# Performance work log

Hardware: AMD Instinct MI355X
Metric: run time of the kernel (lower is better)

The kernel has to match this reference:

```python
import jax, jax.numpy as jnp
import numpy as np

EPS = 1e-5  # torch BatchNorm2d default


def _signature_depth3(path):
    """Truncated (depth-3) path signature via Chen's relation.
    path: [B, P, ch] (P points). Returns [B, ch + ch^2 + ch^3] in signatory
    layout (level 1, then row-major flattened levels 2 and 3)."""
    dx = path[:, 1:] - path[:, :-1]  # [B, P-1, ch] increments
    B, _, ch = dx.shape

    def step(carry, v):
        s1, s2, s3 = carry  # [B,ch], [B,ch,ch], [B,ch,ch,ch]
        vv = v[:, :, None] * v[:, None, :]          # v (x) v
        e2 = 0.5 * vv                               # v^(x)2 / 2!
        e3 = vv[:, :, :, None] * v[:, None, None, :] / 6.0  # v^(x)3 / 3!
        n1 = s1 + v
        n2 = s2 + s1[:, :, None] * v[:, None, :] + e2
        n3 = (s3
              + s2[:, :, :, None] * v[:, None, None, :]
              + s1[:, :, None, None] * e2[:, None, :, :]
              + e3)
        return (n1, n2, n3), None

    init = (jnp.zeros((B, ch), dx.dtype),
            jnp.zeros((B, ch, ch), dx.dtype),
            jnp.zeros((B, ch, ch, ch), dx.dtype))
    (s1, s2, s3), _ = jax.lax.scan(step, init, jnp.transpose(dx, (1, 0, 2)))
    return jnp.concatenate([s1, s2.reshape(B, -1), s3.reshape(B, -1)], axis=1)


def setup_inputs() -> dict:
    key = jax.random.key(0)
    ks = jax.random.split(key, 5)
    N, C, J, T, L = 16, 64, 25, 128, 9
    sic, out_dim = 8, 64
    ch = sic + 1                      # +1 time channel
    sig_ch = ch + ch**2 + ch**3       # 819
    x = jax.random.normal(ks[0], (N, C, J, T, L), jnp.float32)
    conv_w = jax.random.normal(ks[1], (sic, C), jnp.float32) * 0.1
    conv_b = jax.random.normal(ks[2], (sic,), jnp.float32) * 0.1
    bn_gamma = jnp.ones((sic,), jnp.float32)
    bn_beta = jnp.zeros((sic,), jnp.float32)
    lin_w = jax.random.normal(ks[3], (out_dim, sig_ch), jnp.float32) * 0.03
    lin_b = jax.random.normal(ks[4], (out_dim,), jnp.float32) * 0.03
    return dict(x=x, conv_w=conv_w, conv_b=conv_b, bn_gamma=bn_gamma,
                bn_beta=bn_beta, lin_w=lin_w, lin_b=lin_b)


def reference(x, conv_w, conv_b, bn_gamma, bn_beta, lin_w, lin_b):
    N, C, J, T, L = x.shape
    # 1x1 conv over channel dim (applied to [N*L, C, J, T] in torch, which is
    # the same per-position linear map)
    y = jnp.einsum('ncjtl,oc->nojtl', x, conv_w) + conv_b[None, :, None, None, None]
    y = jax.nn.relu(y)
    # BatchNorm2d (training mode): stats over all dims except channel
    mean = y.mean(axis=(0, 2, 3, 4), keepdims=True)
    var = ((y - mean) ** 2).mean(axis=(0, 2, 3, 4), keepdims=True)
    y = ((y - mean) * jax.lax.rsqrt(var + EPS)
         * bn_gamma[None, :, None, None, None] + bn_beta[None, :, None, None, None])
    # -> [N*J*T, L, sic] stream per (n, joint, frame)
    B = N * J * T
    p = jnp.transpose(y, (0, 2, 3, 4, 1)).reshape(B, L, -1)
    # signatory.Augment(include_time=True): prepend time channel in [0, 1]
    t = jnp.broadcast_to(jnp.linspace(0.0, 1.0, L, dtype=x.dtype)[None, :, None], (B, L, 1))
    p = jnp.concatenate([t, p], axis=-1)  # [B, L, ch]
    # signature(..., basepoint=True): prepend zero point
    path = jnp.concatenate([jnp.zeros((B, 1, p.shape[-1]), p.dtype), p], axis=1)
    sig = _signature_depth3(path)          # [B, 819]
    z = sig @ lin_w.T + lin_b              # [B, out_dim]
    return jnp.transpose(z.reshape(N, J, T, -1), (0, 3, 1, 2))  # [N, C, J, T]
```

## Files before the change

kernel.cpp:

```cpp
#include <hip/hip_runtime.h>
#include <hip/hip_bf16.h>

typedef unsigned short u16;
typedef __attribute__((ext_vector_type(8))) short short8;
typedef __attribute__((ext_vector_type(4))) float f32x4;

#define N_    16
#define C_    64
#define J_    25
#define T_    128
#define L_    9
#define SIC   8
#define OUT_  64
#define BTOT  (N_*J_*T_)
#define CNT   (BTOT*L_)
#define KPAD  896
#define NKS   27
#define SPB   28

#define K1C_BLOCKS 900
#define K1BT_BLOCKS 224
#define BT_ELEMS (OUT_*KPAD)

#define PART_OFF  0
#define SS_OFF    16384
#define BT_OFF    32768
#define Y_OFF     65536
#define WS_NEED   ((size_t)(Y_OFF + BTOT*72) * 4)

__device__ __forceinline__ short to_bf16(float x) {
  union { __hip_bfloat16 h; u16 u; } cv;
  cv.h = __float2bfloat16(x);
  return (short)cv.u;
}

__global__ __launch_bounds__(256) void k1_conv(
    const float* __restrict__ x, const float* __restrict__ cw,
    const float* __restrict__ cb, const float* __restrict__ lw,
    float* __restrict__ yws, float* __restrict__ part, u16* __restrict__ Bt) {
  int tid = threadIdx.x;

  if (blockIdx.x >= K1C_BLOCKS) {
    int idx = (blockIdx.x - K1C_BLOCKS) * 256 + tid;
    if (idx < BT_ELEMS) {
      int o = idx / KPAD, k = idx % KPAD;
      float v = 0.f;
      if (k < 864) {
        int i = k / 96, p = k % 96;
        if (p < 91) {
          int orig = (p == 0) ? i : (p < 10 ? 9 + i * 9 + (p - 1) : 90 + i * 81 + (p - 10));
          v = lw[o * 819 + orig];
        }
      }
      Bt[idx] = (u16)to_bf16(v);
    }
    return;
  }

  __shared__ float wlT[C_ * SIC];
  __shared__ float bl[SIC];
  __shared__ float wsum[4][16];
  wlT[tid] = cw[(tid & 7) * C_ + (tid >> 3)];
  wlT[tid + 256] = cw[(tid & 7) * C_ + ((tid + 256) >> 3)];
  if (tid < SIC) bl[tid] = cb[tid];
  __syncthreads();

  int p0 = (blockIdx.x * 256 + tid) * 2;
  int n = p0 / 28800, rem = p0 % 28800;
  int jj = rem / 1152, tl0 = rem % 1152;
  const float* xp = x + (size_t)(n * 1600 + jj) * 1152 + tl0;

  float acc[2][8];
#pragma unroll
  for (int p = 0; p < 2; p++)
#pragma unroll
    for (int o = 0; o < 8; o++) acc[p][o] = bl[o];

#pragma unroll 8
  for (int c = 0; c < C_; c++) {
    float2 xv = *(const float2*)(xp + (size_t)c * 28800);
    float4 w0 = *(const float4*)&wlT[c * 8];
    float4 w1 = *(const float4*)&wlT[c * 8 + 4];
    acc[0][0] = fmaf(xv.x, w0.x, acc[0][0]); acc[1][0] = fmaf(xv.y, w0.x, acc[1][0]);
    acc[0][1] = fmaf(xv.x, w0.y, acc[0][1]); acc[1][1] = fmaf(xv.y, w0.y, acc[1][1]);
    acc[0][2] = fmaf(xv.x, w0.z, acc[0][2]); acc[1][2] = fmaf(xv.y, w0.z, acc[1][2]);
    acc[0][3] = fmaf(xv.x, w0.w, acc[0][3]); acc[1][3] = fmaf(xv.y, w0.w, acc[1][3]);
    acc[0][4] = fmaf(xv.x, w1.x, acc[0][4]); acc[1][4] = fmaf(xv.y, w1.x, acc[1][4]);
    acc[0][5] = fmaf(xv.x, w1.y, acc[0][5]); acc[1][5] = fmaf(xv.y, w1.y, acc[1][5]);
    acc[0][6] = fmaf(xv.x, w1.z, acc[0][6]); acc[1][6] = fmaf(xv.y, w1.z, acc[1][6]);
    acc[0][7] = fmaf(xv.x, w1.w, acc[0][7]); acc[1][7] = fmaf(xv.y, w1.w, acc[1][7]);
  }

  float vals[16];
#pragma unroll
  for (int q = 0; q < 16; q++) vals[q] = 0.f;
  float4* dst = (float4*)(yws + (size_t)p0 * 8);
#pragma unroll
  for (int p = 0; p < 2; p++) {
#pragma unroll
    for (int o = 0; o < 8; o++) acc[p][o] = fmaxf(acc[p][o], 0.f);
    dst[p * 2]     = make_float4(acc[p][0], acc[p][1], acc[p][2], acc[p][3]);
    dst[p * 2 + 1] = make_float4(acc[p][4], acc[p][5], acc[p][6], acc[p][7]);
#pragma unroll
    for (int o = 0; o < 8; o++) {
      vals[o] += acc[p][o];
      vals[8 + o] += acc[p][o] * acc[p][o];
    }
  }

  int lane = tid & 63, wid = tid >> 6;
#pragma unroll
  for (int v = 0; v < 16; v++) {
    float s = vals[v];
    for (int off = 32; off > 0; off >>= 1) s += __shfl_down(s, off, 64);
    if (lane == 0) wsum[wid][v] = s;
  }
  __syncthreads();
  if (tid < 16)
    part[blockIdx.x * 16 + tid] = wsum[0][tid] + wsum[1][tid] + wsum[2][tid] + wsum[3][tid];
}

__global__ __launch_bounds__(256) void k2_stats(
    const float* __restrict__ part, const float* __restrict__ gamma,
    const float* __restrict__ beta, float* __restrict__ ss) {
  __shared__ float red[16][16];
  int tid = threadIdx.x;
  int val = tid & 15, grp = tid >> 4;
  float s0 = 0.f, s1 = 0.f, s2 = 0.f, s3 = 0.f;
  int b = grp;
  for (; b + 48 < K1C_BLOCKS; b += 64) {
    s0 += part[b * 16 + val];
    s1 += part[(b + 16) * 16 + val];
    s2 += part[(b + 32) * 16 + val];
    s3 += part[(b + 48) * 16 + val];
  }
  for (; b < K1C_BLOCKS; b += 16) s0 += part[b * 16 + val];
  red[grp][val] = (s0 + s1) + (s2 + s3);
  __syncthreads();
  if (tid < 16) {
    float tot = 0.f;
#pragma unroll
    for (int g = 0; g < 16; g++) tot += red[g][tid];
    red[0][tid] = tot;
  }
  __syncthreads();
  if (tid < 8) {
    float mean = red[0][tid] * (1.f / CNT);
    float var  = red[0][8 + tid] * (1.f / CNT) - mean * mean;
    float sc = gamma[tid] * rsqrtf(var + 1e-5f);
    ss[tid] = sc;
    ss[8 + tid] = beta[tid] - mean * sc;
  }
}

__global__ __launch_bounds__(256, 3) void k3_fused(
    const float* __restrict__ yws, const float* __restrict__ ss,
    const u16* __restrict__ Bt, const float* __restrict__ lb,
    float* __restrict__ out) {
  __shared__ __align__(16) u16 sig_lds[29 * KPAD];
  __shared__ float ssl[16];
  __shared__ float lbl[64];
  float* ylds = (float*)sig_lds;
  int tid = threadIdx.x;
  if (tid < 16) ssl[tid] = ss[tid];
  if (tid >= 64 && tid < 128) lbl[tid - 64] = lb[tid - 64];
  int gBase = blockIdx.x * SPB;
  int valid = BTOT - gBase; if (valid > SPB) valid = SPB;
  __syncthreads();

  if (tid < SPB * 9) {
    int s = tid / 9;
    if (s < valid) {
      const float4* src = (const float4*)(yws + (size_t)gBase * 72 + (size_t)tid * 8);
      float4 a = src[0], b = src[1];
      float* drow = ylds + tid * 8;
      drow[0] = fmaf(a.x, ssl[0], ssl[8]);
      drow[1] = fmaf(a.y, ssl[1], ssl[9]);
      drow[2] = fmaf(a.z, ssl[2], ssl[10]);
      drow[3] = fmaf(a.w, ssl[3], ssl[11]);
      drow[4] = fmaf(b.x, ssl[4], ssl[12]);
      drow[5] = fmaf(b.y, ssl[5], ssl[13]);
      drow[6] = fmaf(b.z, ssl[6], ssl[14]);
      drow[7] = fmaf(b.w, ssl[7], ssl[15]);
    }
  }
  {
    short8 z = {0, 0, 0, 0, 0, 0, 0, 0};
    int padChunks = (29 - valid) * 112;
    for (int e = tid; e < padChunks; e += 256) {
      int r = valid + e / 112, sl = e % 112;
      *(short8*)&sig_lds[r * KPAD + sl * 8] = z;
    }
  }
  __syncthreads();

  int s = tid / 9, i = tid % 9;
  bool act = (tid < SPB * 9) && (s < valid);
  float s1 = 0.f, s2[9], s3[81];
#pragma unroll
  for (int jj = 0; jj < 9; jj++) s2[jj] = 0.f;
#pragma unroll
  for (int q = 0; q < 81; q++) s3[q] = 0.f;
  if (act) {
    const float* yrow = ylds + s * 72;
    int i1 = (i == 0) ? 0 : (i - 1);
    float prev[8], prevvi = 0.f;
#pragma unroll
    for (int c = 0; c < 8; c++) prev[c] = 0.f;

#pragma unroll 3
    for (int l = 0; l < 9; l++) {
      float4 a4 = *(const float4*)(yrow + l * 8);
      float4 b4 = *(const float4*)(yrow + l * 8 + 4);
      float ldsv = yrow[l * 8 + i1];
      float cur[8] = {a4.x, a4.y, a4.z, a4.w, b4.x, b4.y, b4.z, b4.w};
      float v[9];
      v[0] = (l == 0) ? 0.f : 0.125f;
#pragma unroll
      for (int c = 0; c < 8; c++) v[c + 1] = cur[c] - prev[c];
      float curvi = (i == 0) ? (float)l * 0.125f : ldsv;
      float vi = curvi - prevvi;
      prevvi = curvi;
      float aa = fmaf(vi, (1.f / 6.f), 0.5f * s1);
      float b2 = fmaf(vi, 0.5f, s1);
#pragma unroll
      for (int jj = 0; jj < 9; jj++) {
        float tj = fmaf(aa, v[jj], s2[jj]);
#pragma unroll
        for (int k = 0; k < 9; k++) s3[jj * 9 + k] = fmaf(tj, v[k], s3[jj * 9 + k]);
        s2[jj] = fmaf(b2, v[jj], s2[jj]);
      }
      s1 += vi;
#pragma unroll
      for (int c = 0; c < 8; c++) prev[c] = cur[c];
    }
  }
  __syncthreads();

  if (act) {
    u16* rowbase = sig_lds + s * KPAD;
    int sw = s & 7;
    {
      short8 ch;
      ch[0] = to_bf16(s1);
#pragma unroll
      for (int w = 0; w < 7; w++) ch[w + 1] = to_bf16(s2[w]);
      *(short8*)&rowbase[(((i * 12 + 0) ^ sw) * 8)] = ch;
    }
    {
      short8 ch;
      ch[0] = to_bf16(s2[7]); ch[1] = to_bf16(s2[8]);
#pragma unroll
      for (int w = 0; w < 6; w++) ch[w + 2] = to_bf16(s3[w]);
      *(short8*)&rowbase[(((i * 12 + 1) ^ sw) * 8)] = ch;
    }
#pragma unroll
    for (int c = 2; c <= 10; c++) {
      short8 ch;
#pragma unroll
      for (int w = 0; w < 8; w++) ch[w] = to_bf16(s3[c * 8 - 10 + w]);
      *(short8*)&rowbase[(((i * 12 + c) ^ sw) * 8)] = ch;
    }
    {
      short8 ch;
      ch[0] = to_bf16(s3[78]); ch[1] = to_bf16(s3[79]); ch[2] = to_bf16(s3[80]);
      ch[3] = 0; ch[4] = 0; ch[5] = 0; ch[6] = 0; ch[7] = 0;
      *(short8*)&rowbase[(((i * 12 + 11) ^ sw) * 8)] = ch;
    }
  }
  __syncthreads();

  int w = tid >> 6, l = tid & 63;
  int brow = (w << 4) + (l & 15);
  const short8* bp = (const short8*)(Bt + (size_t)brow * KPAD);
  int arow0 = (l & 15);
  int arow1 = 16 + (l & 15); if (arow1 > 28) arow1 = 28;
  int asw0 = arow0 & 7, asw1 = arow1 & 7;
  f32x4 acc0 = {0, 0, 0, 0}, acc1 = {0, 0, 0, 0};
#pragma unroll
  for (int ks = 0; ks < NKS; ks++) {
    int s4 = ks * 4 + (l >> 4);
    short8 bfrag = bp[s4];
    short8 a0 = *(const short8*)&sig_lds[arow0 * KPAD + ((s4 ^ asw0) * 8)];
    short8 a1 = *(const short8*)&sig_lds[arow1 * KPAD + ((s4 ^ asw1) * 8)];
    acc0 = __builtin_amdgcn_mfma_f32_16x16x32_bf16(a0, bfrag, acc0, 0, 0, 0);
    acc1 = __builtin_amdgcn_mfma_f32_16x16x32_bf16(a1, bfrag, acc1, 0, 0, 0);
  }
  __syncthreads();

  float* c_lds = (float*)sig_lds;
  int o = (w << 4) + (l & 15);
#pragma unroll
  for (int r = 0; r < 4; r++) {
    int m0 = (l >> 4) * 4 + r;
    c_lds[o * 33 + m0] = acc0[r];
    c_lds[o * 33 + 16 + m0] = acc1[r];
  }
  __syncthreads();
  for (int e = tid; e < 2048; e += 256) {
    int o2 = e >> 5, m = e & 31;
    if (m < valid) {
      int b = gBase + m;
      int n = b / (J_ * T_), rem = b % (J_ * T_);
      int j = rem >> 7, t = rem & (T_ - 1);
      out[(((size_t)n * OUT_ + o2) * J_ + j) * T_ + t] = c_lds[o2 * 33 + m] + lbl[o2];
    }
  }
}

extern "C" void kernel_launch(void* const* d_in, const int* in_sizes, int n_in,
                              void* d_out, int out_size, void* d_ws, size_t ws_size,
                              hipStream_t stream) {
  const float* x     = (const float*)d_in[0];
  const float* cw    = (const float*)d_in[1];
  const float* cb    = (const float*)d_in[2];
  const float* gamma = (const float*)d_in[3];
  const float* beta  = (const float*)d_in[4];
  const float* lw    = (const float*)d_in[5];
  const float* lbias = (const float*)d_in[6];
  float* out = (float*)d_out;
  float* ws  = (float*)d_ws;
  if (ws_size < WS_NEED) return;

  float* part = ws + PART_OFF;
  float* ss   = ws + SS_OFF;
  u16*   bt   = (u16*)(ws + BT_OFF);
  float* yws  = ws + Y_OFF;

  hipLaunchKernelGGL(k1_conv, dim3(K1C_BLOCKS + K1BT_BLOCKS), dim3(256), 0, stream,
                     x, cw, cb, lw, yws, part, bt);
  hipLaunchKernelGGL(k2_stats, dim3(1), dim3(256), 0, stream, part, gamma, beta, ss);

  int nblk3 = (BTOT + SPB - 1) / SPB;
  hipLaunchKernelGGL(k3_fused, dim3(nblk3), dim3(256), 0, stream, yws, ss, bt, lbias, out);
}
```

Measured before the change: 70.82 us.

## Halve conv block size, use nontemporal x loads and packed bf16 conversion

```diff
diff --git a/kernel.cpp b/kernel.cpp
--- a/kernel.cpp
+++ b/kernel.cpp
@@ -4,6 +4,8 @@
 typedef unsigned short u16;
 typedef __attribute__((ext_vector_type(8))) short short8;
 typedef __attribute__((ext_vector_type(4))) float f32x4;
+typedef __attribute__((ext_vector_type(2))) float f32x2;
+typedef __attribute__((ext_vector_type(4))) unsigned int u32x4;
 
 #define N_    16
 #define C_    64
@@ -18,15 +20,22 @@
 #define NKS   27
 #define SPB   28
 
-#define K1C_BLOCKS 900
-#define K1BT_BLOCKS 224
-#define BT_ELEMS (OUT_*KPAD)
+#define K1_TPB     128
+#define K1C_BLOCKS 1800
+#define BT_ELEMS   (OUT_*KPAD)
+#define K1BT_BLOCKS (BT_ELEMS / K1_TPB)
 
 #define PART_OFF  0
-#define SS_OFF    16384
-#define BT_OFF    32768
-#define Y_OFF     65536
+#define SS_OFF    32768
+#define BT_OFF    40960
+#define Y_OFF     69632
 #define WS_NEED   ((size_t)(Y_OFF + BTOT*72) * 4)
+
+__device__ __forceinline__ unsigned pkbf(float a, float b) {
+  unsigned r;
+  asm("v_cvt_pk_bf16_f32 %0, %1, %2" : "=v"(r) : "v"(a), "v"(b));
+  return r;
+}
 
 __device__ __forceinline__ short to_bf16(float x) {
   union { __hip_bfloat16 h; u16 u; } cv;
@@ -34,38 +43,36 @@
   return (short)cv.u;
 }
 
-__global__ __launch_bounds__(256) void k1_conv(
+__global__ __launch_bounds__(K1_TPB) void k1_conv(
     const float* __restrict__ x, const float* __restrict__ cw,
     const float* __restrict__ cb, const float* __restrict__ lw,
     float* __restrict__ yws, float* __restrict__ part, u16* __restrict__ Bt) {
   int tid = threadIdx.x;
 
   if (blockIdx.x >= K1C_BLOCKS) {
-    int idx = (blockIdx.x - K1C_BLOCKS) * 256 + tid;
-    if (idx < BT_ELEMS) {
-      int o = idx / KPAD, k = idx % KPAD;
-      float v = 0.f;
-      if (k < 864) {
-        int i = k / 96, p = k % 96;
-        if (p < 91) {
-          int orig = (p == 0) ? i : (p < 10 ? 9 + i * 9 + (p - 1) : 90 + i * 81 + (p - 10));
-          v = lw[o * 819 + orig];
-        }
+    int idx = (blockIdx.x - K1C_BLOCKS) * K1_TPB + tid;
+    int o = idx / KPAD, k = idx % KPAD;
+    float v = 0.f;
+    if (k < 864) {
+      int i = k / 96, p = k % 96;
+      if (p < 91) {
+        int orig = (p == 0) ? i : (p < 10 ? 9 + i * 9 + (p - 1) : 90 + i * 81 + (p - 10));
+        v = lw[o * 819 + orig];
       }
-      Bt[idx] = (u16)to_bf16(v);
-    }
+    }
+    Bt[idx] = (u16)to_bf16(v);
     return;
   }
 
   __shared__ float wlT[C_ * SIC];
   __shared__ float bl[SIC];
-  __shared__ float wsum[4][16];
-  wlT[tid] = cw[(tid & 7) * C_ + (tid >> 3)];
-  wlT[tid + 256] = cw[(tid & 7) * C_ + ((tid + 256) >> 3)];
+  __shared__ float wsum[2][16];
+  for (int q = tid; q < C_ * SIC; q += K1_TPB)
+    wlT[q] = cw[(q & 7) * C_ + (q >> 3)];
   if (tid < SIC) bl[tid] = cb[tid];
   __syncthreads();
 
-  int p0 = (blockIdx.x * 256 + tid) * 2;
+  int p0 = (blockIdx.x * K1_TPB + tid) * 2;
   int n = p0 / 28800, rem = p0 % 28800;
   int jj = rem / 1152, tl0 = rem % 1152;
   const float* xp = x + (size_t)(n * 1600 + jj) * 1152 + tl0;
@@ -78,17 +85,17 @@
 
 #pragma unroll 8
   for (int c = 0; c < C_; c++) {
-    float2 xv = *(const float2*)(xp + (size_t)c * 28800);
+    f32x2 xv = __builtin_nontemporal_load((const f32x2*)(xp + (size_t)c * 28800));
     float4 w0 = *(const float4*)&wlT[c * 8];
     float4 w1 = *(const float4*)&wlT[c * 8 + 4];
-    acc[0][0] = fmaf(xv.x, w0.x, acc[0][0]); acc[1][0] = fmaf(xv.y, w0.x, acc[1][0]);
-    acc[0][1] = fmaf(xv.x, w0.y, acc[0][1]); acc[1][1] = fmaf(xv.y, w0.y, acc[1][1]);
-    acc[0][2] = fmaf(xv.x, w0.z, acc[0][2]); acc[1][2] = fmaf(xv.y, w0.z, acc[1][2]);
-    acc[0][3] = fmaf(xv.x, w0.w, acc[0][3]); acc[1][3] = fmaf(xv.y, w0.w, acc[1][3]);
-    acc[0][4] = fmaf(xv.x, w1.x, acc[0][4]); acc[1][4] = fmaf(xv.y, w1.x, acc[1][4]);
-    acc[0][5] = fmaf(xv.x, w1.y, acc[0][5]); acc[1][5] = fmaf(xv.y, w1.y, acc[1][5]);
-    acc[0][6] = fmaf(xv.x, w1.z, acc[0][6]); acc[1][6] = fmaf(xv.y, w1.z, acc[1][6]);
-    acc[0][7] = fmaf(xv.x, w1.w, acc[0][7]); acc[1][7] = fmaf(xv.y, w1.w, acc[1][7]);
+    acc[0][0] = fmaf(xv[0], w0.x, acc[0][0]); acc[1][0] = fmaf(xv[1], w0.x, acc[1][0]);
+    acc[0][1] = fmaf(xv[0], w0.y, acc[0][1]); acc[1][1] = fmaf(xv[1], w0.y, acc[1][1]);
+    acc[0][2] = fmaf(xv[0], w0.z, acc[0][2]); acc[1][2] = fmaf(xv[1], w0.z, acc[1][2]);
+    acc[0][3] = fmaf(xv[0], w0.w, acc[0][3]); acc[1][3] = fmaf(xv[1], w0.w, acc[1][3]);
+    acc[0][4] = fmaf(xv[0], w1.x, acc[0][4]); acc[1][4] = fmaf(xv[1], w1.x, acc[1][4]);
+    acc[0][5] = fmaf(xv[0], w1.y, acc[0][5]); acc[1][5] = fmaf(xv[1], w1.y, acc[1][5]);
+    acc[0][6] = fmaf(xv[0], w1.z, acc[0][6]); acc[1][6] = fmaf(xv[1], w1.z, acc[1][6]);
+    acc[0][7] = fmaf(xv[0], w1.w, acc[0][7]); acc[1][7] = fmaf(xv[1], w1.w, acc[1][7]);
   }
 
   float vals[16];
@@ -117,7 +124,7 @@
   }
   __syncthreads();
   if (tid < 16)
-    part[blockIdx.x * 16 + tid] = wsum[0][tid] + wsum[1][tid] + wsum[2][tid] + wsum[3][tid];
+    part[blockIdx.x * 16 + tid] = wsum[0][tid] + wsum[1][tid];
 }
 
 __global__ __launch_bounds__(256) void k2_stats(
@@ -126,16 +133,16 @@
   __shared__ float red[16][16];
   int tid = threadIdx.x;
   int val = tid & 15, grp = tid >> 4;
-  float s0 = 0.f, s1 = 0.f, s2 = 0.f, s3 = 0.f;
+  float s[8];
+#pragma unroll
+  for (int q = 0; q < 8; q++) s[q] = 0.f;
   int b = grp;
-  for (; b + 48 < K1C_BLOCKS; b += 64) {
-    s0 += part[b * 16 + val];
-    s1 += part[(b + 16) * 16 + val];
-    s2 += part[(b + 32) * 16 + val];
-    s3 += part[(b + 48) * 16 + val];
-  }
-  for (; b < K1C_BLOCKS; b += 16) s0 += part[b * 16 + val];
-  red[grp][val] = (s0 + s1) + (s2 + s3);
+  for (; b + 112 < K1C_BLOCKS; b += 128) {
+#pragma unroll
+    for (int q = 0; q < 8; q++) s[q] += part[(b + q * 16) * 16 + val];
+  }
+  for (; b < K1C_BLOCKS; b += 16) s[0] += part[b * 16 + val];
+  red[grp][val] = ((s[0] + s[1]) + (s[2] + s[3])) + ((s[4] + s[5]) + (s[6] + s[7]));
   __syncthreads();
   if (tid < 16) {
     float tot = 0.f;
@@ -241,31 +248,36 @@
     u16* rowbase = sig_lds + s * KPAD;
     int sw = s & 7;
     {
-      short8 ch;
-      ch[0] = to_bf16(s1);
-#pragma unroll
-      for (int w = 0; w < 7; w++) ch[w + 1] = to_bf16(s2[w]);
-      *(short8*)&rowbase[(((i * 12 + 0) ^ sw) * 8)] = ch;
+      u32x4 ch;
+      ch[0] = pkbf(s1, s2[0]);    ch[1] = pkbf(s2[1], s2[2]);
+      ch[2] = pkbf(s2[3], s2[4]); ch[3] = pkbf(s2[5], s2[6]);
+      *(u32x4*)&rowbase[(((i * 12 + 0) ^ sw) * 8)] = ch;
     }
     {
-      short8 ch;
-      ch[0] = to_bf16(s2[7]); ch[1] = to_bf16(s2[8]);
-#pragma unroll
-      for (int w = 0; w < 6; w++) ch[w + 2] = to_bf16(s3[w]);
-      *(short8*)&rowbase[(((i * 12 + 1) ^ sw) * 8)] = ch;
+      u32x4 ch;
+      ch[0] = pkbf(s2[7], s2[8]); ch[1] = pkbf(s3[0], s3[1]);
+      ch[2] = pkbf(s3[2], s3[3]); ch[3] = pkbf(s3[4], s3[5]);
+      *(u32x4*)&rowbase[(((i * 12 + 1) ^ sw) * 8)] = ch;
     }
 #pragma unroll
     for (int c = 2; c <= 10; c++) {
-      short8 ch;
-#pragma unroll
-      for (int w = 0; w < 8; w++) ch[w] = to_bf16(s3[c * 8 - 10 + w]);
-      *(short8*)&rowbase[(((i * 12 + c) ^ sw) * 8)] = ch;
+      int base = c * 8 - 10;
+      u32x4 ch;
+      ch[0] = pkbf(s3[base],     s3[base + 1]);
+      ch[1] = pkbf(s3[base + 2], s3[base + 3]);
+      ch[2] = pkbf(s3[base + 4], s3[base + 5]);
+      ch[3] = pkbf(s3[base + 6], s3[base + 7]);
+      *(u32x4*)&rowbase[(((i * 12 + c) ^ sw) * 8)] = ch;
     }
     {
-      short8 ch;
-      ch[0] = to_bf16(s3[78]); ch[1] = to_bf16(s3[79]); ch[2] = to_bf16(s3[80]);
-      ch[3] = 0; ch[4] = 0; ch[5] = 0; ch[6] = 0; ch[7] = 0;
-      *(short8*)&rowbase[(((i * 12 + 11) ^ sw) * 8)] = ch;
+      u32x4 ch;
+      ch[0] = pkbf(s3[78], s3[79]); ch[1] = pkbf(s3[80], 0.f);
+      ch[2] = 0u; ch[3] = 0u;
+      *(u32x4*)&rowbase[(((i * 12 + 11) ^ sw) * 8)] = ch;
+    }
+    if (i < 4) {
+      u32x4 z = {0u, 0u, 0u, 0u};
+      *(u32x4*)&rowbase[(((108 + i) ^ sw) * 8)] = z;
     }
   }
   __syncthreads();
@@ -327,7 +339,7 @@
   u16*   bt   = (u16*)(ws + BT_OFF);
   float* yws  = ws + Y_OFF;
 
-  hipLaunchKernelGGL(k1_conv, dim3(K1C_BLOCKS + K1BT_BLOCKS), dim3(256), 0, stream,
+  hipLaunchKernelGGL(k1_conv, dim3(K1C_BLOCKS + K1BT_BLOCKS), dim3(K1_TPB), 0, stream,
                      x, cw, cb, lw, yws, part, bt);
   hipLaunchKernelGGL(k2_stats, dim3(1), dim3(256), 0, stream, part, gamma, beta, ss);
 
```

Result: slower. 75.41 us (+6.5%).
